# Kernel optimization log

Measured on AMD Instinct MI355X. Metric: run time of the kernel, lower is better.

The kernel has to match this reference:

```python
import jax, jax.numpy as jnp
import numpy as np

N_SEL = 8192
N_FEAT = 256
K_SUB = 256
N_PERS = 4
E_FULL = 262144
E_RAW = 262144
N_TOTAL = 8192
EPSILON = 0.5
LAMB1 = 0.5


def setup_inputs() -> dict:
    key = jax.random.key(0)
    ks = jax.random.split(key, 8)
    x = jax.random.normal(ks[0], (N_SEL, N_FEAT), dtype=jnp.float32)
    metric_weight = jax.random.uniform(ks[1], (N_PERS, N_FEAT), dtype=jnp.float32)
    selected_batch = jnp.sort(jax.random.randint(ks[2], (N_SEL,), 0, K_SUB, dtype=jnp.int32))
    selected_mapping = jax.random.randint(ks[3], (N_SEL,), 0, N_TOTAL, dtype=jnp.int32)
    selected_belong = jax.random.randint(ks[4], (K_SUB,), 0, K_SUB, dtype=jnp.int32)
    selected_score = jax.random.uniform(ks[5], (K_SUB,), dtype=jnp.float32)
    full_edge_index = jax.random.randint(ks[6], (2, E_FULL), 0, N_SEL, dtype=jnp.int32)
    raw_edge_index = jax.random.randint(ks[7], (2, E_RAW), 0, N_TOTAL, dtype=jnp.int32)
    return {"x": x, "metric_weight": metric_weight, "selected_batch": selected_batch,
            "selected_mapping": selected_mapping, "selected_belong": selected_belong,
            "selected_score": selected_score, "full_edge_index": full_edge_index,
            "raw_edge_index": raw_edge_index, "n_total": N_TOTAL}


def weighted_cosine(x, w):
    # x: [N, D], w: [P, D] -> mean over P perspectives of cosine sim
    h = x[None, :, :] * w[:, None, :]                        # [P, N, D]
    h = h / (jnp.linalg.norm(h, axis=-1, keepdims=True) + 1e-12)
    return jnp.einsum('pnd,pmd->nm', h, h) / w.shape[0]      # [N, N]


def reference(x, metric_weight, selected_batch, selected_mapping, selected_belong,
              selected_score, full_edge_index, raw_edge_index, n_total):
    n_sel = x.shape[0]
    k_sub = selected_score.shape[0]
    # scatter score normalization: scores of subgraphs sharing a 'belong' group sum to 1
    score_sum = jax.ops.segment_sum(selected_score, selected_belong, num_segments=k_sub)
    score = selected_score / score_sum[selected_belong]
    # z_node = x (no encoder); weighted-cosine metric over all selected nodes
    adj = weighted_cosine(x, metric_weight)                  # [N_sel, N_sel]
    # mask to allowed intra-subgraph edges (full_edge_index)
    mask = jnp.zeros_like(adj).at[full_edge_index[0], full_edge_index[1]].set(1.0)
    adj = adj * mask
    # postprocess: EpsilonNN threshold, then remove self loops
    adj = adj * (adj > EPSILON).astype(adj.dtype)
    diag = jnp.arange(n_sel)
    adj = adj.at[diag, diag].set(0.0)
    # per-edge weight = normalized score of the source node's subgraph, times lamb1
    adj_w = adj * (score[selected_batch] * LAMB1)[:, None]
    # map selected-node indices to global node ids and coalesce (sum duplicates)
    tmp = jnp.zeros((n_total, n_sel), adj.dtype).at[selected_mapping].add(adj_w)
    out = jnp.zeros((n_total, n_total), adj.dtype).at[:, selected_mapping].add(tmp)
    # add raw graph with weight (1 - lamb1); coalesce == dense scatter-add
    out = out.at[raw_edge_index[0], raw_edge_index[1]].add(1.0 - LAMB1)
    return out
```

## Files before the change

### kernel.cpp

```cpp
#include <hip/hip_runtime.h>

typedef float f4 __attribute__((ext_vector_type(4)));

#define N_SEL   8192
#define N_FEAT  256
#define K_SUB   256
#define N_PERS  4
#define E_FULL  262144
#define E_RAW   262144
#define N_TOTAL 8192
#define EPSILON 0.5f
#define LAMB1   0.5f

#define WS_SCORE_OFF  (128 * 1024)
#define WS_CNT_OFF    (132 * 1024)
#define WS_XQ_OFF     (256 * 1024)
#define WS_LIST_OFF   (WS_XQ_OFF + 2 * 1024 * 1024)

__global__ __launch_bounds__(256) void prep_kernel(const f4* __restrict__ x4,
                                                   const f4* __restrict__ w4,
                                                   f4* __restrict__ invn4,
                                                   unsigned int* __restrict__ xq,
                                                   const float* __restrict__ s,
                                                   const int* __restrict__ belong,
                                                   float* __restrict__ score,
                                                   int* __restrict__ cnt) {
    __shared__ float sv[K_SUB];
    __shared__ int bv[K_SUB];
    int gid = blockIdx.x * 256 + threadIdx.x;
    int n = gid >> 6;
    int lane = threadIdx.x & 63;

    f4 xv = x4[(size_t)n * 64 + lane];

    int pk = 0;
    pk = __builtin_amdgcn_cvt_pk_fp8_f32(xv.x, xv.y, pk, false);
    pk = __builtin_amdgcn_cvt_pk_fp8_f32(xv.z, xv.w, pk, true);
    xq[(size_t)n * 64 + lane] = (unsigned int)pk;

    f4 ssv;
    #pragma unroll
    for (int p = 0; p < 4; ++p) {
        f4 h = xv * w4[p * 64 + lane];
        float ss = h.x * h.x + h.y * h.y + h.z * h.z + h.w * h.w;
        #pragma unroll
        for (int off = 32; off; off >>= 1) ss += __shfl_xor(ss, off);
        ssv[p] = ss;
    }
    if (lane == 0) {
        f4 r;
        r.x = 1.0f / (sqrtf(ssv.x) + 1e-12f);
        r.y = 1.0f / (sqrtf(ssv.y) + 1e-12f);
        r.z = 1.0f / (sqrtf(ssv.z) + 1e-12f);
        r.w = 1.0f / (sqrtf(ssv.w) + 1e-12f);
        invn4[n] = r;
    }

    if (gid == 0) *cnt = 0;

    if (blockIdx.x == 0) {
        int t = threadIdx.x;
        sv[t] = s[t];
        bv[t] = belong[t];
        __syncthreads();
        int myb = bv[t];
        float sum = 0.0f;
        for (int k = 0; k < K_SUB; ++k)
            if (bv[k] == myb) sum += sv[k];
        score[t] = sv[t] / sum;
    }
}

__global__ __launch_bounds__(256) void zero_edge_kernel(f4* __restrict__ out4,
                                                        const unsigned int* __restrict__ xq,
                                                        const f4* __restrict__ w4,
                                                        const int* __restrict__ fe,
                                                        const int* __restrict__ sel_batch,
                                                        const f4* __restrict__ invn4,
                                                        const float* __restrict__ score,
                                                        int2* __restrict__ list,
                                                        int* __restrict__ cnt) {
    int b = blockIdx.x;
    int t = threadIdx.x;
    int lane = t & 63;
    int w = t >> 6;

    int ebase = b * 128 + w * 32;
    int myidx = (lane < 32) ? fe[ebase + lane] : fe[E_FULL + ebase + (lane - 32)];

    f4 q0 = w4[0 * 64 + lane]; q0 *= q0;
    f4 q1 = w4[1 * 64 + lane]; q1 *= q1;
    f4 q2 = w4[2 * 64 + lane]; q2 *= q2;
    f4 q3 = w4[3 * 64 + lane]; q3 *= q3;

    int rowid = b * 4 + w;
    size_t obase = (size_t)rowid * 2048;
    f4 z = (f4)0.0f;

    int ci = __shfl(myidx, 0);
    int cj = __shfl(myidx, 32);
    unsigned int xi = xq[(size_t)ci * 64 + lane];
    unsigned int xj = xq[(size_t)cj * 64 + lane];
    f4 ii = invn4[ci];
    f4 ij = invn4[cj];

    #pragma unroll 4
    for (int s = 0; s < 32; ++s) {
        int i = ci, j = cj;
        unsigned int ax = xi, bx = xj;
        f4 aii = ii, aij = ij;

        if (s < 31) {
            ci = __shfl(myidx, s + 1);
            cj = __shfl(myidx, 32 + s + 1);
            xi = xq[(size_t)ci * 64 + lane];
            xj = xq[(size_t)cj * 64 + lane];
            ii = invn4[ci];
            ij = invn4[cj];
        }
        __builtin_amdgcn_sched_barrier(0);

        out4[obase + s * 64 + lane] = z;

        float pd0 = __builtin_amdgcn_cvt_f32_fp8((int)ax, 0) *
                    __builtin_amdgcn_cvt_f32_fp8((int)bx, 0);
        float pd1 = __builtin_amdgcn_cvt_f32_fp8((int)ax, 1) *
                    __builtin_amdgcn_cvt_f32_fp8((int)bx, 1);
        float pd2 = __builtin_amdgcn_cvt_f32_fp8((int)ax, 2) *
                    __builtin_amdgcn_cvt_f32_fp8((int)bx, 2);
        float pd3 = __builtin_amdgcn_cvt_f32_fp8((int)ax, 3) *
                    __builtin_amdgcn_cvt_f32_fp8((int)bx, 3);

        float a0 = fmaf(pd3, q0.w, fmaf(pd2, q0.z, fmaf(pd1, q0.y, pd0 * q0.x)));
        float a1 = fmaf(pd3, q1.w, fmaf(pd2, q1.z, fmaf(pd1, q1.y, pd0 * q1.x)));
        float a2 = fmaf(pd3, q2.w, fmaf(pd2, q2.z, fmaf(pd1, q2.y, pd0 * q2.x)));
        float a3 = fmaf(pd3, q3.w, fmaf(pd2, q3.z, fmaf(pd1, q3.y, pd0 * q3.x)));

        float v = a0 * (aii.x * aij.x) + a1 * (aii.y * aij.y) +
                  a2 * (aii.z * aij.z) + a3 * (aii.w * aij.w);
        v += __shfl_xor(v, 1);
        v += __shfl_xor(v, 2);
        v += __shfl_xor(v, 4);
        v += __shfl_xor(v, 8);
        v += __shfl_xor(v, 16);
        v += __shfl_xor(v, 32);

        if (lane == 0 && i != j) {
            v *= 0.25f;
            if (v > EPSILON) {
                float val = v * score[sel_batch[i]] * LAMB1;
                int idx = atomicAdd(cnt, 1);
                int2 ent;
                ent.x = (i << 13) | j;
                ent.y = __float_as_int(val);
                list[idx] = ent;
            }
        }
    }
}

__global__ __launch_bounds__(256) void raw_finalize_kernel(const int* __restrict__ re,
                                                           const int2* __restrict__ list,
                                                           const int* __restrict__ cnt,
                                                           const int* __restrict__ sel_map,
                                                           float* __restrict__ out) {
    int t = blockIdx.x * 256 + threadIdx.x;
    if (t < E_RAW) {
        int u = re[t];
        int v = re[E_RAW + t];
        atomicAdd(&out[(size_t)u * N_TOTAL + v], 1.0f - LAMB1);
    }
    int n = *cnt;
    if (t < n) {
        int2 ek = list[t];
        bool first = true;
        for (int l = 0; l < t; ++l)
            if (list[l].x == ek.x) { first = false; break; }
        if (first) {
            int i = ek.x >> 13;
            int j = ek.x & (N_SEL - 1);
            atomicAdd(&out[(size_t)sel_map[i] * N_TOTAL + sel_map[j]],
                      __int_as_float(ek.y));
        }
    }
}

extern "C" void kernel_launch(void* const* d_in, const int* in_sizes, int n_in,
                              void* d_out, int out_size, void* d_ws, size_t ws_size,
                              hipStream_t stream) {
    const float* x         = (const float*)d_in[0];
    const float* mw        = (const float*)d_in[1];
    const int* sel_batch   = (const int*)d_in[2];
    const int* sel_map     = (const int*)d_in[3];
    const int* sel_belong  = (const int*)d_in[4];
    const float* sel_score = (const float*)d_in[5];
    const int* fe          = (const int*)d_in[6];
    const int* re          = (const int*)d_in[7];
    float* out             = (float*)d_out;

    char* ws         = (char*)d_ws;
    f4* invn4        = (f4*)ws;
    float* score     = (float*)(ws + WS_SCORE_OFF);
    int* cnt         = (int*)(ws + WS_CNT_OFF);
    unsigned int* xq = (unsigned int*)(ws + WS_XQ_OFF);
    int2* list       = (int2*)(ws + WS_LIST_OFF);

    prep_kernel<<<2048, 256, 0, stream>>>(
        (const f4*)x, (const f4*)mw, invn4, xq, sel_score, sel_belong, score, cnt);
    zero_edge_kernel<<<2048, 256, 0, stream>>>(
        (f4*)out, xq, (const f4*)mw, fe, sel_batch,
        invn4, score, list, cnt);
    raw_finalize_kernel<<<1024, 256, 0, stream>>>(re, list, cnt, sel_map, out);
}
```

Measured before the change: 92.06 us.

## Split output zeroing into separate kernel and fuse raw-edge scatter into edge kernel

Zeroing of the 256MB output moves out of the edge-similarity kernel into a dedicated streaming zero kernel. The raw-edge atomic scatter moves into the edge kernel, which can do it now that zeroing already happened in an earlier launch. The finalize kernel only handles the deduplicated selected-edge list. This trades the interleaved store/compute overlap for a pure bandwidth-bound memset plus lighter edge kernel, and adds one extra launch.

```diff
diff --git a/kernel.cpp b/kernel.cpp
--- a/kernel.cpp
+++ b/kernel.cpp
@@ -71,19 +71,35 @@
     }
 }
 
-__global__ __launch_bounds__(256) void zero_edge_kernel(f4* __restrict__ out4,
-                                                        const unsigned int* __restrict__ xq,
-                                                        const f4* __restrict__ w4,
-                                                        const int* __restrict__ fe,
-                                                        const int* __restrict__ sel_batch,
-                                                        const f4* __restrict__ invn4,
-                                                        const float* __restrict__ score,
-                                                        int2* __restrict__ list,
-                                                        int* __restrict__ cnt) {
+__global__ __launch_bounds__(256) void zero_kernel(f4* __restrict__ p) {
+    int gid = blockIdx.x * 256 + threadIdx.x;
+    f4 z = (f4)0.0f;
+    #pragma unroll
+    for (int k = 0; k < 16; ++k)
+        p[(size_t)k * 1048576 + gid] = z;
+}
+
+__global__ __launch_bounds__(256) void edge_raw_kernel(float* __restrict__ out,
+                                                       const unsigned int* __restrict__ xq,
+                                                       const f4* __restrict__ w4,
+                                                       const int* __restrict__ fe,
+                                                       const int* __restrict__ re,
+                                                       const int* __restrict__ sel_batch,
+                                                       const f4* __restrict__ invn4,
+                                                       const float* __restrict__ score,
+                                                       int2* __restrict__ list,
+                                                       int* __restrict__ cnt) {
     int b = blockIdx.x;
     int t = threadIdx.x;
+    int gt = b * 256 + t;
     int lane = t & 63;
     int w = t >> 6;
+
+    if (gt < E_RAW) {
+        int u = re[gt];
+        int v = re[E_RAW + gt];
+        atomicAdd(&out[(size_t)u * N_TOTAL + v], 1.0f - LAMB1);
+    }
 
     int ebase = b * 128 + w * 32;
     int myidx = (lane < 32) ? fe[ebase + lane] : fe[E_FULL + ebase + (lane - 32)];
@@ -92,10 +108,6 @@
     f4 q1 = w4[1 * 64 + lane]; q1 *= q1;
     f4 q2 = w4[2 * 64 + lane]; q2 *= q2;
     f4 q3 = w4[3 * 64 + lane]; q3 *= q3;
-
-    int rowid = b * 4 + w;
-    size_t obase = (size_t)rowid * 2048;
-    f4 z = (f4)0.0f;
 
     int ci = __shfl(myidx, 0);
     int cj = __shfl(myidx, 32);
@@ -109,7 +121,6 @@
         int i = ci, j = cj;
         unsigned int ax = xi, bx = xj;
         f4 aii = ii, aij = ij;
-
         if (s < 31) {
             ci = __shfl(myidx, s + 1);
             cj = __shfl(myidx, 32 + s + 1);
@@ -118,9 +129,6 @@
             ii = invn4[ci];
             ij = invn4[cj];
         }
-        __builtin_amdgcn_sched_barrier(0);
-
-        out4[obase + s * 64 + lane] = z;
 
         float pd0 = __builtin_amdgcn_cvt_f32_fp8((int)ax, 0) *
                     __builtin_amdgcn_cvt_f32_fp8((int)bx, 0);
@@ -159,30 +167,19 @@
     }
 }
 
-__global__ __launch_bounds__(256) void raw_finalize_kernel(const int* __restrict__ re,
-                                                           const int2* __restrict__ list,
-                                                           const int* __restrict__ cnt,
-                                                           const int* __restrict__ sel_map,
-                                                           float* __restrict__ out) {
+__global__ __launch_bounds__(256) void finalize_kernel(const int2* __restrict__ list,
+                                                       const int* __restrict__ cnt,
+                                                       const int* __restrict__ sel_map,
+                                                       float* __restrict__ out) {
     int t = blockIdx.x * 256 + threadIdx.x;
-    if (t < E_RAW) {
-        int u = re[t];
-        int v = re[E_RAW + t];
-        atomicAdd(&out[(size_t)u * N_TOTAL + v], 1.0f - LAMB1);
-    }
     int n = *cnt;
-    if (t < n) {
-        int2 ek = list[t];
-        bool first = true;
-        for (int l = 0; l < t; ++l)
-            if (list[l].x == ek.x) { first = false; break; }
-        if (first) {
-            int i = ek.x >> 13;
-            int j = ek.x & (N_SEL - 1);
-            atomicAdd(&out[(size_t)sel_map[i] * N_TOTAL + sel_map[j]],
-                      __int_as_float(ek.y));
-        }
-    }
+    if (t >= n) return;
+    int2 ek = list[t];
+    for (int l = 0; l < t; ++l)
+        if (list[l].x == ek.x) return;
+    int i = ek.x >> 13;
+    int j = ek.x & (N_SEL - 1);
+    atomicAdd(&out[(size_t)sel_map[i] * N_TOTAL + sel_map[j]], __int_as_float(ek.y));
 }
 
 extern "C" void kernel_launch(void* const* d_in, const int* in_sizes, int n_in,
@@ -207,8 +204,8 @@
 
     prep_kernel<<<2048, 256, 0, stream>>>(
         (const f4*)x, (const f4*)mw, invn4, xq, sel_score, sel_belong, score, cnt);
-    zero_edge_kernel<<<2048, 256, 0, stream>>>(
-        (f4*)out, xq, (const f4*)mw, fe, sel_batch,
-        invn4, score, list, cnt);
-    raw_finalize_kernel<<<1024, 256, 0, stream>>>(re, list, cnt, sel_map, out);
-}
+    zero_kernel<<<4096, 256, 0, stream>>>((f4*)out);
+    edge_raw_kernel<<<2048, 256, 0, stream>>>(
+        out, xq, (const f4*)mw, fe, re, sel_batch, invn4, score, list, cnt);
+    finalize_kernel<<<E_FULL / 256, 256, 0, stream>>>(list, cnt, sel_map, out);
+}
```

Result: slower. 110.0 us (+19.5%).
